# Performance work log

Measured on AMD Instinct MI355X. Metric: run time of the kernel, lower is better.

## Reference

```python
import jax, jax.numpy as jnp
import numpy as np

N_NODES = 100000
N_EDGES = 1600000
IN_DIM = 128
HID = 64


def setup_inputs() -> dict:
    key = jax.random.key(0)
    ks = jax.random.split(key, 12)
    s = 1.0 / np.sqrt(IN_DIM)
    sh = 1.0 / np.sqrt(HID)
    return {
        "x": jax.random.normal(ks[0], (N_NODES, IN_DIM), jnp.float32),
        "edge_index": jax.random.randint(ks[1], (2, N_EDGES), 0, N_NODES, jnp.int64)
        if jax.config.jax_enable_x64 else jax.random.randint(ks[1], (2, N_EDGES), 0, N_NODES, jnp.int32),
        "edge_attr": jax.random.uniform(ks[2], (N_EDGES, 1), jnp.float32),
        "Wi": jax.random.normal(ks[3], (IN_DIM, HID), jnp.float32) * s,
        "bi": jnp.zeros((HID,), jnp.float32),
        "W1": jax.random.normal(ks[4], (HID, HID), jnp.float32) * sh,
        "b1": jnp.zeros((HID,), jnp.float32),
        "W2": jax.random.normal(ks[5], (HID, HID), jnp.float32) * sh,
        "b2": jnp.zeros((HID,), jnp.float32),
        "W3": jax.random.normal(ks[6], (HID, HID), jnp.float32) * sh,
        "b3": jnp.zeros((HID,), jnp.float32),
    }


def reference(x, edge_index, edge_attr, Wi, bi, W1, b1, W2, b2, W3, b3):
    src = edge_index[0]
    tgt = edge_index[1]
    w = edge_attr[:, 0:1]  # [E,1]
    h = jax.nn.relu(x @ Wi + bi)  # [N,H]
    states = [h]
    for W, b in ((W1, b1), (W2, b2), (W3, b3)):
        # per-edge weighted message, scatter-add into target nodes
        msgs = jax.ops.segment_sum(h[src] * w, tgt, num_segments=h.shape[0])
        h = jax.nn.relu((h + msgs) @ W + b)
        states.append(h)
    return jnp.stack(states)  # [4, N, H] (list of states in the original)
```

## Files before the change

### kernel.cpp

```cpp
#include <hip/hip_runtime.h>
#include <hip/hip_bf16.h>

#define N_NODES 100000
#define N_EDGES 1600000
#define IN_DIM  128
#define HID     64
#define BIN_NODES 64
#define NBINS   ((N_NODES + BIN_NODES - 1) / BIN_NODES)
#define EB      2048
#define EB_BLOCKS ((N_EDGES + EB - 1) / EB)
#define CAP     2048

#define PITCH_IN  152
#define PITCH_HID 88

typedef __attribute__((ext_vector_type(8))) short bf16x8;
typedef __attribute__((ext_vector_type(4))) float f32x4;

__device__ inline unsigned short f2bf(float f) {
    __hip_bfloat16 b = __float2bfloat16(f);
    return *reinterpret_cast<unsigned short*>(&b);
}

__global__ void wf_prep_kernel(const float* __restrict__ Wi,
                               const float* __restrict__ W1,
                               const float* __restrict__ W2,
                               const float* __restrict__ W3,
                               unsigned short* __restrict__ wf_in,
                               unsigned short* __restrict__ wf_hid,
                               int* __restrict__ g_bin_cursor) {
    int t = blockIdx.x * 256 + threadIdx.x;
    if (t < NBINS) g_bin_cursor[t] = t * CAP;
    if (t < 8192) {
        int j = t & 7, n16 = (t >> 3) & 15, quad = (t >> 7) & 3, nt = (t >> 9) & 3, kc = t >> 11;
        int k = kc * 32 + quad * 8 + j, n = nt * 16 + n16;
        wf_in[t] = f2bf(Wi[k * HID + n]);
    }
    if (t < 4096) {
        int j = t & 7, n16 = (t >> 3) & 15, quad = (t >> 7) & 3, nt = (t >> 9) & 3, kc = t >> 11;
        int k = kc * 32 + quad * 8 + j, n = nt * 16 + n16;
        wf_hid[t]        = f2bf(W1[k * HID + n]);
        wf_hid[4096 + t] = f2bf(W2[k * HID + n]);
        wf_hid[8192 + t] = f2bf(W3[k * HID + n]);
    }
}

struct ScatterS {
    unsigned long long srec[EB];
    unsigned short sbin[EB];
    int cnt[NBINS];
    int lstart[NBINS];
    int lbase[NBINS];
    int stot;
};
struct GemmS {
    unsigned short sX[64 * PITCH_IN];
};

__global__ __launch_bounds__(256) void fused_prep_kernel(
        const int* __restrict__ src,
        const int* __restrict__ tgt,
        const float* __restrict__ ea,
        int* __restrict__ g_bin_cursor,
        unsigned long long* __restrict__ binned,
        const float* __restrict__ x,
        const unsigned short* __restrict__ wf,
        const float* __restrict__ bi,
        float* __restrict__ h0,
        __hip_bfloat16* __restrict__ hbf) {
    __shared__ __align__(16) unsigned char smem[sizeof(ScatterS)];
    const int tid = threadIdx.x;

    if (blockIdx.x < EB_BLOCKS) {
        ScatterS* S = reinterpret_cast<ScatterS*>(smem);
        for (int i = tid; i < NBINS; i += 256) S->cnt[i] = 0;
        __syncthreads();

        const int e0 = blockIdx.x * EB;
        int myb[EB / 256];
        unsigned long long myrec[EB / 256];
        #pragma unroll
        for (int i = 0; i < EB / 256; ++i) {
            int e = e0 + tid + i * 256;
            if (e < N_EDGES) {
                int t = tgt[e];
                int b = t >> 6;
                myb[i] = b;
                myrec[i] = ((unsigned long long)(unsigned)__float_as_int(ea[e]) << 32)
                         | ((unsigned)(t & 63) << 17) | (unsigned)src[e];
                atomicAdd(&S->cnt[b], 1);
            } else {
                myb[i] = -1;
            }
        }
        __syncthreads();

        if (tid < 64) {
            int carry = 0;
            for (int c = 0; c < (NBINS + 63) / 64; ++c) {
                int idx = c * 64 + tid;
                int v = (idx < NBINS) ? S->cnt[idx] : 0;
                int sc = v;
                #pragma unroll
                for (int d = 1; d < 64; d <<= 1) {
                    int t2 = __shfl_up(sc, d);
                    if (tid >= d) sc += t2;
                }
                if (idx < NBINS) S->lstart[idx] = carry + sc - v;
                carry += __shfl(sc, 63);
            }
            if (tid == 0) S->stot = carry;
        }
        __syncthreads();

        for (int i = tid; i < NBINS; i += 256)
            if (S->cnt[i]) S->lbase[i] = atomicAdd(&g_bin_cursor[i], S->cnt[i]);
        __syncthreads();
        for (int i = tid; i < NBINS; i += 256) S->cnt[i] = 0;
        __syncthreads();

        #pragma unroll
        for (int i = 0; i < EB / 256; ++i) {
            if (myb[i] >= 0) {
                int r = atomicAdd(&S->cnt[myb[i]], 1);
                int p = S->lstart[myb[i]] + r;
                S->srec[p] = myrec[i];
                S->sbin[p] = (unsigned short)myb[i];
            }
        }
        __syncthreads();

        const int tot = S->stot;
        for (int i = tid; i < tot; i += 256) {
            int b = S->sbin[i];
            binned[(size_t)S->lbase[b] + (i - S->lstart[b])] = S->srec[i];
        }
    } else {
        GemmS* G = reinterpret_cast<GemmS*>(smem);
        const int row0 = (blockIdx.x - EB_BLOCKS) * 64;

        #pragma unroll
        for (int it = 0; it < 8; ++it) {
            int i  = tid + it * 256;
            int r  = i >> 5;
            int kq = i & 31;
            int rg = row0 + r;
            float4 v = (rg < N_NODES)
                     ? ((const float4*)x)[(size_t)rg * (IN_DIM / 4) + kq]
                     : make_float4(0.f, 0.f, 0.f, 0.f);
            ushort4 pk;
            pk.x = f2bf(v.x); pk.y = f2bf(v.y); pk.z = f2bf(v.z); pk.w = f2bf(v.w);
            *(ushort4*)(G->sX + r * PITCH_IN + kq * 4) = pk;
        }
        __syncthreads();

        const int lane = tid & 63;
        const int wid  = tid >> 6;
        const int l16  = lane & 15;
        const int q    = lane >> 4;

        f32x4 acc[4] = {{0,0,0,0},{0,0,0,0},{0,0,0,0},{0,0,0,0}};
        const bf16x8* wf8 = (const bf16x8*)wf;

        #pragma unroll
        for (int kc = 0; kc < 4; ++kc) {
            bf16x8 af = *(const bf16x8*)(G->sX + (wid * 16 + l16) * PITCH_IN + kc * 32 + q * 8);
            #pragma unroll
            for (int nt = 0; nt < 4; ++nt) {
                bf16x8 bfr = wf8[((kc * 4 + nt) * 4 + q) * 16 + l16];
                acc[nt] = __builtin_amdgcn_mfma_f32_16x16x32_bf16(af, bfr, acc[nt], 0, 0, 0);
            }
        }

        #pragma unroll
        for (int nt = 0; nt < 4; ++nt) {
            float bb = bi[nt * 16 + l16];
            #pragma unroll
            for (int reg = 0; reg < 4; ++reg) {
                int rg = row0 + wid * 16 + q * 4 + reg;
                if (rg < N_NODES) {
                    float v = fmaxf(acc[nt][reg] + bb, 0.0f);
                    h0 [(size_t)rg * HID + nt * 16 + l16] = v;
                    hbf[(size_t)rg * HID + nt * 16 + l16] = __float2bfloat16(v);
                }
            }
        }
    }
}

__global__ __launch_bounds__(256) void agg_gemm_kernel(
        const float* __restrict__ h,
        const __hip_bfloat16* __restrict__ hbf_in,
        const int* __restrict__ g_bin_cursor,
        const unsigned long long* __restrict__ binned,
        const unsigned short* __restrict__ wf,
        const float* __restrict__ b,
        float* __restrict__ hnext,
        __hip_bfloat16* __restrict__ hbf_out,
        const int store_bf) {
    __shared__ int2 sp[CAP];
    __shared__ unsigned short sXs[64 * PITCH_HID];
    __shared__ int nbase[64], ncur[64], scnt[64];
    const int tid  = threadIdx.x;
    const int bin  = blockIdx.x;
    const int row0 = bin * 64;
    const int lane = tid & 63;
    const int wid  = tid >> 6;
    const int grp  = lane >> 4;
    const int sub  = lane & 15;
    const int ebeg = bin * CAP;
    const int ecnt = g_bin_cursor[bin] - ebeg;

    if (tid < 64) ncur[tid] = 0;
    __syncthreads();
    for (int i = tid; i < ecnt; i += 256)
        atomicAdd(&ncur[(int)((binned[ebeg + i] >> 17) & 63)], 1);
    __syncthreads();

    if (tid < 64) {
        int v = ncur[tid], sc = v;
        #pragma unroll
        for (int d = 1; d < 64; d <<= 1) {
            int t2 = __shfl_up(sc, d);
            if (tid >= d) sc += t2;
        }
        nbase[tid] = sc - v;
        scnt[tid]  = v;
        ncur[tid]  = sc - v;
    }
    __syncthreads();

    for (int i = tid; i < ecnt; i += 256) {
        unsigned long long rec = binned[ebeg + i];
        int lt = (int)((rec >> 17) & 63);
        int r  = atomicAdd(&ncur[lt], 1);
        sp[r] = make_int2((int)(rec & 0x1FFFF), (int)(rec >> 32));
    }
    __syncthreads();

    for (int t = 0; t < 16; ++t) {
        const int lt   = wid * 16 + t;
        const int node = row0 + lt;
        if (node < N_NODES) {
            const int beg = nbase[lt];
            const int cnt = scnt[lt];
            float ax = 0.f, ay = 0.f, az = 0.f, aw = 0.f;
            const int last = cnt - 1;
            for (int i = 0; i < cnt; i += 8) {
                int e0 = i + grp;
                int e1 = i + 4 + grp;
                bool l0 = (e0 <= last);
                bool l1 = (e1 <= last);
                int2 p0 = sp[beg + (l0 ? e0 : last)];
                int2 p1 = sp[beg + (l1 ? e1 : last)];
                uint2 g0 = *(const uint2*)(hbf_in + (size_t)p0.x * HID + sub * 4);
                uint2 g1 = *(const uint2*)(hbf_in + (size_t)p1.x * HID + sub * 4);
                float w0 = l0 ? __int_as_float(p0.y) : 0.0f;
                float w1 = l1 ? __int_as_float(p1.y) : 0.0f;
                ax += w0 * __uint_as_float(g0.x << 16);
                ay += w0 * __uint_as_float(g0.x & 0xFFFF0000u);
                az += w0 * __uint_as_float(g0.y << 16);
                aw += w0 * __uint_as_float(g0.y & 0xFFFF0000u);
                ax += w1 * __uint_as_float(g1.x << 16);
                ay += w1 * __uint_as_float(g1.x & 0xFFFF0000u);
                az += w1 * __uint_as_float(g1.y << 16);
                aw += w1 * __uint_as_float(g1.y & 0xFFFF0000u);
            }
            ax += __shfl_xor(ax, 16); ay += __shfl_xor(ay, 16);
            az += __shfl_xor(az, 16); aw += __shfl_xor(aw, 16);
            ax += __shfl_xor(ax, 32); ay += __shfl_xor(ay, 32);
            az += __shfl_xor(az, 32); aw += __shfl_xor(aw, 32);
            if (grp == 0) {
                const float4 hv = *(const float4*)(h + (size_t)node * HID + sub * 4);
                ushort4 pk;
                pk.x = f2bf(hv.x + ax); pk.y = f2bf(hv.y + ay);
                pk.z = f2bf(hv.z + az); pk.w = f2bf(hv.w + aw);
                *(ushort4*)(sXs + lt * PITCH_HID + sub * 4) = pk;
            }
        } else if (grp == 0) {
            ushort4 z; z.x = 0; z.y = 0; z.z = 0; z.w = 0;
            *(ushort4*)(sXs + lt * PITCH_HID + sub * 4) = z;
        }
    }
    __syncthreads();

    const int l16 = lane & 15;
    const int q   = lane >> 4;

    f32x4 acc[4] = {{0,0,0,0},{0,0,0,0},{0,0,0,0},{0,0,0,0}};
    const bf16x8* wf8 = (const bf16x8*)wf;

    #pragma unroll
    for (int kc = 0; kc < 2; ++kc) {
        bf16x8 af = *(const bf16x8*)(sXs + (wid * 16 + l16) * PITCH_HID + kc * 32 + q * 8);
        #pragma unroll
        for (int nt = 0; nt < 4; ++nt) {
            bf16x8 bfr = wf8[((kc * 4 + nt) * 4 + q) * 16 + l16];
            acc[nt] = __builtin_amdgcn_mfma_f32_16x16x32_bf16(af, bfr, acc[nt], 0, 0, 0);
        }
    }

    #pragma unroll
    for (int nt = 0; nt < 4; ++nt) {
        float bb = b[nt * 16 + l16];
        #pragma unroll
        for (int reg = 0; reg < 4; ++reg) {
            int rg = row0 + wid * 16 + q * 4 + reg;
            if (rg < N_NODES) {
                float v = fmaxf(acc[nt][reg] + bb, 0.0f);
                hnext[(size_t)rg * HID + nt * 16 + l16] = v;
                if (store_bf)
                    hbf_out[(size_t)rg * HID + nt * 16 + l16] = __float2bfloat16(v);
            }
        }
    }
}

extern "C" void kernel_launch(void* const* d_in, const int* in_sizes, int n_in,
                              void* d_out, int out_size, void* d_ws, size_t ws_size,
                              hipStream_t stream) {
    const float* x   = (const float*)d_in[0];
    const int*   ei  = (const int*)  d_in[1];
    const float* ea  = (const float*)d_in[2];
    const float* Wi  = (const float*)d_in[3];
    const float* bi  = (const float*)d_in[4];
    const float* W1  = (const float*)d_in[5];
    const float* b1  = (const float*)d_in[6];
    const float* W2  = (const float*)d_in[7];
    const float* b2  = (const float*)d_in[8];
    const float* W3  = (const float*)d_in[9];
    const float* b3  = (const float*)d_in[10];
    const float* bl[3] = { b1, b2, b3 };
    float* out = (float*)d_out;

    const int* src = ei;
    const int* tgt = ei + N_EDGES;

    unsigned long long* binned = (unsigned long long*)d_ws;
    int* g_bin_cursor = (int*)(binned + (size_t)NBINS * CAP);
    __hip_bfloat16* hbf0 = (__hip_bfloat16*)(g_bin_cursor + NBINS + 1);
    __hip_bfloat16* hbf1 = hbf0 + (size_t)N_NODES * HID;
    unsigned short* wf_in  = (unsigned short*)(hbf1 + (size_t)N_NODES * HID);
    unsigned short* wf_hid = wf_in + 8192;

    wf_prep_kernel<<<32, 256, 0, stream>>>(Wi, W1, W2, W3, wf_in, wf_hid,
                                           g_bin_cursor);

    const int gemm_blocks = (N_NODES + 63) / 64;
    fused_prep_kernel<<<EB_BLOCKS + gemm_blocks, 256, 0, stream>>>(
        src, tgt, ea, g_bin_cursor, binned,
        x, wf_in, bi, out, hbf0);

    __hip_bfloat16* hin  = hbf0;
    __hip_bfloat16* hout = hbf1;
    for (int l = 0; l < 3; ++l) {
        const float* hl = out + (size_t)l * N_NODES * HID;
        float* hn       = out + (size_t)(l + 1) * N_NODES * HID;
        agg_gemm_kernel<<<NBINS, 256, 0, stream>>>(
            hl, hin, g_bin_cursor, binned,
            wf_hid + (size_t)l * 4096, bl[l], hn, hout, (l < 2) ? 1 : 0);
        __hip_bfloat16* t = hin; hin = hout; hout = t;
    }
}
```

Baseline: 419.3 us.

## Replace two-level bin sort with direct per-node edge slots via global atomics

Edges are no longer radix-binned into 64-node bins in shared memory and then re-sorted by node inside every aggregation layer. A single scatter kernel now uses one global atomic per edge to place (src, weight) records into a fixed 64-slot row per target node. The aggregation kernel reads each node's slots with one wavefront load, prefetches the next node's row, and hands out edges through lane shuffles instead of an LDS list. This removes the per-layer in-block sorting and LDS staging, at the cost of scattered global atomics and a larger sparse workspace. Any edges beyond 64 per node are silently dropped, and the input GEMM no longer runs in the same launch as the scatter.

```diff
diff --git a/kernel.cpp b/kernel.cpp
--- a/kernel.cpp
+++ b/kernel.cpp
@@ -5,11 +5,7 @@
 #define N_EDGES 1600000
 #define IN_DIM  128
 #define HID     64
-#define BIN_NODES 64
-#define NBINS   ((N_NODES + BIN_NODES - 1) / BIN_NODES)
-#define EB      2048
-#define EB_BLOCKS ((N_EDGES + EB - 1) / EB)
-#define CAP     2048
+#define CAP_N   64
 
 #define PITCH_IN  152
 #define PITCH_HID 88
@@ -28,9 +24,9 @@
                                const float* __restrict__ W3,
                                unsigned short* __restrict__ wf_in,
                                unsigned short* __restrict__ wf_hid,
-                               int* __restrict__ g_bin_cursor) {
+                               int* __restrict__ cnt) {
     int t = blockIdx.x * 256 + threadIdx.x;
-    if (t < NBINS) g_bin_cursor[t] = t * CAP;
+    if (t < N_NODES) cnt[t] = 0;
     if (t < 8192) {
         int j = t & 7, n16 = (t >> 3) & 15, quad = (t >> 7) & 3, nt = (t >> 9) & 3, kc = t >> 11;
         int k = kc * 32 + quad * 8 + j, n = nt * 16 + n16;
@@ -45,144 +41,74 @@
     }
 }
 
-struct ScatterS {
-    unsigned long long srec[EB];
-    unsigned short sbin[EB];
-    int cnt[NBINS];
-    int lstart[NBINS];
-    int lbase[NBINS];
-    int stot;
-};
-struct GemmS {
-    unsigned short sX[64 * PITCH_IN];
-};
-
-__global__ __launch_bounds__(256) void fused_prep_kernel(
+__global__ __launch_bounds__(256) void scatter_direct_kernel(
         const int* __restrict__ src,
         const int* __restrict__ tgt,
         const float* __restrict__ ea,
-        int* __restrict__ g_bin_cursor,
-        unsigned long long* __restrict__ binned,
+        int* __restrict__ cnt,
+        int2* __restrict__ binned) {
+    int e = blockIdx.x * 256 + threadIdx.x;
+    if (e < N_EDGES) {
+        int t = tgt[e];
+        int r = atomicAdd(&cnt[t], 1);
+        if (r < CAP_N)
+            binned[(size_t)t * CAP_N + r] = make_int2(src[e], __float_as_int(ea[e]));
+    }
+}
+
+__global__ __launch_bounds__(256) void gemm_in_kernel(
         const float* __restrict__ x,
         const unsigned short* __restrict__ wf,
         const float* __restrict__ bi,
         float* __restrict__ h0,
         __hip_bfloat16* __restrict__ hbf) {
-    __shared__ __align__(16) unsigned char smem[sizeof(ScatterS)];
-    const int tid = threadIdx.x;
-
-    if (blockIdx.x < EB_BLOCKS) {
-        ScatterS* S = reinterpret_cast<ScatterS*>(smem);
-        for (int i = tid; i < NBINS; i += 256) S->cnt[i] = 0;
-        __syncthreads();
-
-        const int e0 = blockIdx.x * EB;
-        int myb[EB / 256];
-        unsigned long long myrec[EB / 256];
-        #pragma unroll
-        for (int i = 0; i < EB / 256; ++i) {
-            int e = e0 + tid + i * 256;
-            if (e < N_EDGES) {
-                int t = tgt[e];
-                int b = t >> 6;
-                myb[i] = b;
-                myrec[i] = ((unsigned long long)(unsigned)__float_as_int(ea[e]) << 32)
-                         | ((unsigned)(t & 63) << 17) | (unsigned)src[e];
-                atomicAdd(&S->cnt[b], 1);
-            } else {
-                myb[i] = -1;
-            }
-        }
-        __syncthreads();
-
-        if (tid < 64) {
-            int carry = 0;
-            for (int c = 0; c < (NBINS + 63) / 64; ++c) {
-                int idx = c * 64 + tid;
-                int v = (idx < NBINS) ? S->cnt[idx] : 0;
-                int sc = v;
-                #pragma unroll
-                for (int d = 1; d < 64; d <<= 1) {
-                    int t2 = __shfl_up(sc, d);
-                    if (tid >= d) sc += t2;
-                }
-                if (idx < NBINS) S->lstart[idx] = carry + sc - v;
-                carry += __shfl(sc, 63);
-            }
-            if (tid == 0) S->stot = carry;
-        }
-        __syncthreads();
-
-        for (int i = tid; i < NBINS; i += 256)
-            if (S->cnt[i]) S->lbase[i] = atomicAdd(&g_bin_cursor[i], S->cnt[i]);
-        __syncthreads();
-        for (int i = tid; i < NBINS; i += 256) S->cnt[i] = 0;
-        __syncthreads();
-
-        #pragma unroll
-        for (int i = 0; i < EB / 256; ++i) {
-            if (myb[i] >= 0) {
-                int r = atomicAdd(&S->cnt[myb[i]], 1);
-                int p = S->lstart[myb[i]] + r;
-                S->srec[p] = myrec[i];
-                S->sbin[p] = (unsigned short)myb[i];
-            }
-        }
-        __syncthreads();
-
-        const int tot = S->stot;
-        for (int i = tid; i < tot; i += 256) {
-            int b = S->sbin[i];
-            binned[(size_t)S->lbase[b] + (i - S->lstart[b])] = S->srec[i];
-        }
-    } else {
-        GemmS* G = reinterpret_cast<GemmS*>(smem);
-        const int row0 = (blockIdx.x - EB_BLOCKS) * 64;
-
-        #pragma unroll
-        for (int it = 0; it < 8; ++it) {
-            int i  = tid + it * 256;
-            int r  = i >> 5;
-            int kq = i & 31;
-            int rg = row0 + r;
-            float4 v = (rg < N_NODES)
-                     ? ((const float4*)x)[(size_t)rg * (IN_DIM / 4) + kq]
-                     : make_float4(0.f, 0.f, 0.f, 0.f);
-            ushort4 pk;
-            pk.x = f2bf(v.x); pk.y = f2bf(v.y); pk.z = f2bf(v.z); pk.w = f2bf(v.w);
-            *(ushort4*)(G->sX + r * PITCH_IN + kq * 4) = pk;
-        }
-        __syncthreads();
-
-        const int lane = tid & 63;
-        const int wid  = tid >> 6;
-        const int l16  = lane & 15;
-        const int q    = lane >> 4;
-
-        f32x4 acc[4] = {{0,0,0,0},{0,0,0,0},{0,0,0,0},{0,0,0,0}};
-        const bf16x8* wf8 = (const bf16x8*)wf;
-
-        #pragma unroll
-        for (int kc = 0; kc < 4; ++kc) {
-            bf16x8 af = *(const bf16x8*)(G->sX + (wid * 16 + l16) * PITCH_IN + kc * 32 + q * 8);
-            #pragma unroll
-            for (int nt = 0; nt < 4; ++nt) {
-                bf16x8 bfr = wf8[((kc * 4 + nt) * 4 + q) * 16 + l16];
-                acc[nt] = __builtin_amdgcn_mfma_f32_16x16x32_bf16(af, bfr, acc[nt], 0, 0, 0);
-            }
-        }
-
+    __shared__ unsigned short sX[64 * PITCH_IN];
+    const int tid  = threadIdx.x;
+    const int row0 = blockIdx.x * 64;
+
+    #pragma unroll
+    for (int it = 0; it < 8; ++it) {
+        int i  = tid + it * 256;
+        int r  = i >> 5;
+        int kq = i & 31;
+        int rg = row0 + r;
+        float4 v = (rg < N_NODES)
+                 ? ((const float4*)x)[(size_t)rg * (IN_DIM / 4) + kq]
+                 : make_float4(0.f, 0.f, 0.f, 0.f);
+        ushort4 pk;
+        pk.x = f2bf(v.x); pk.y = f2bf(v.y); pk.z = f2bf(v.z); pk.w = f2bf(v.w);
+        *(ushort4*)(sX + r * PITCH_IN + kq * 4) = pk;
+    }
+    __syncthreads();
+
+    const int lane = tid & 63;
+    const int wid  = tid >> 6;
+    const int l16  = lane & 15;
+    const int q    = lane >> 4;
+
+    f32x4 acc[4] = {{0,0,0,0},{0,0,0,0},{0,0,0,0},{0,0,0,0}};
+    const bf16x8* wf8 = (const bf16x8*)wf;
+
+    #pragma unroll
+    for (int kc = 0; kc < 4; ++kc) {
+        bf16x8 af = *(const bf16x8*)(sX + (wid * 16 + l16) * PITCH_IN + kc * 32 + q * 8);
         #pragma unroll
         for (int nt = 0; nt < 4; ++nt) {
-            float bb = bi[nt * 16 + l16];
-            #pragma unroll
-            for (int reg = 0; reg < 4; ++reg) {
-                int rg = row0 + wid * 16 + q * 4 + reg;
-                if (rg < N_NODES) {
-                    float v = fmaxf(acc[nt][reg] + bb, 0.0f);
-                    h0 [(size_t)rg * HID + nt * 16 + l16] = v;
-                    hbf[(size_t)rg * HID + nt * 16 + l16] = __float2bfloat16(v);
-                }
+            bf16x8 bfr = wf8[((kc * 4 + nt) * 4 + q) * 16 + l16];
+            acc[nt] = __builtin_amdgcn_mfma_f32_16x16x32_bf16(af, bfr, acc[nt], 0, 0, 0);
+        }
+    }
+
+    #pragma unroll
+    for (int nt = 0; nt < 4; ++nt) {
+        float bb = bi[nt * 16 + l16];
+        #pragma unroll
+        for (int reg = 0; reg < 4; ++reg) {
+            int rg = row0 + wid * 16 + q * 4 + reg;
+            if (rg < N_NODES) {
+                float v = fmaxf(acc[nt][reg] + bb, 0.0f);
+                h0 [(size_t)rg * HID + nt * 16 + l16] = v;
+                hbf[(size_t)rg * HID + nt * 16 + l16] = __float2bfloat16(v);
             }
         }
     }
@@ -191,72 +117,57 @@
 __global__ __launch_bounds__(256) void agg_gemm_kernel(
         const float* __restrict__ h,
         const __hip_bfloat16* __restrict__ hbf_in,
-        const int* __restrict__ g_bin_cursor,
-        const unsigned long long* __restrict__ binned,
+        const int* __restrict__ cnt,
+        const int2* __restrict__ binned,
         const unsigned short* __restrict__ wf,
         const float* __restrict__ b,
         float* __restrict__ hnext,
         __hip_bfloat16* __restrict__ hbf_out,
         const int store_bf) {
-    __shared__ int2 sp[CAP];
     __shared__ unsigned short sXs[64 * PITCH_HID];
-    __shared__ int nbase[64], ncur[64], scnt[64];
     const int tid  = threadIdx.x;
-    const int bin  = blockIdx.x;
-    const int row0 = bin * 64;
+    const int row0 = blockIdx.x * 64;
     const int lane = tid & 63;
     const int wid  = tid >> 6;
     const int grp  = lane >> 4;
     const int sub  = lane & 15;
-    const int ebeg = bin * CAP;
-    const int ecnt = g_bin_cursor[bin] - ebeg;
-
-    if (tid < 64) ncur[tid] = 0;
-    __syncthreads();
-    for (int i = tid; i < ecnt; i += 256)
-        atomicAdd(&ncur[(int)((binned[ebeg + i] >> 17) & 63)], 1);
-    __syncthreads();
-
-    if (tid < 64) {
-        int v = ncur[tid], sc = v;
-        #pragma unroll
-        for (int d = 1; d < 64; d <<= 1) {
-            int t2 = __shfl_up(sc, d);
-            if (tid >= d) sc += t2;
-        }
-        nbase[tid] = sc - v;
-        scnt[tid]  = v;
-        ncur[tid]  = sc - v;
-    }
-    __syncthreads();
-
-    for (int i = tid; i < ecnt; i += 256) {
-        unsigned long long rec = binned[ebeg + i];
-        int lt = (int)((rec >> 17) & 63);
-        int r  = atomicAdd(&ncur[lt], 1);
-        sp[r] = make_int2((int)(rec & 0x1FFFF), (int)(rec >> 32));
-    }
-    __syncthreads();
+
+    const int node0 = row0 + wid * 16;
+
+    int cv = 0;
+    {
+        int nl = node0 + (lane & 15);
+        if (lane < 16 && nl < N_NODES) cv = min(cnt[nl], CAP_N);
+    }
+
+    int c0 = __shfl(cv, 0);
+    int2 pl = binned[(size_t)min(node0, N_NODES - 1) * CAP_N + min(lane, max(c0 - 1, 0))];
 
     for (int t = 0; t < 16; ++t) {
-        const int lt   = wid * 16 + t;
-        const int node = row0 + lt;
+        const int node = node0 + t;
+        const int ccur = __shfl(cv, t);
+        const int2 pl_cur = pl;
+        if (t < 15) {
+            int cn = __shfl(cv, t + 1);
+            pl = binned[(size_t)min(node + 1, N_NODES - 1) * CAP_N
+                        + min(lane, max(cn - 1, 0))];
+        }
         if (node < N_NODES) {
-            const int beg = nbase[lt];
-            const int cnt = scnt[lt];
             float ax = 0.f, ay = 0.f, az = 0.f, aw = 0.f;
-            const int last = cnt - 1;
-            for (int i = 0; i < cnt; i += 8) {
+            const int last = ccur - 1;
+            for (int i = 0; i < ccur; i += 8) {
                 int e0 = i + grp;
                 int e1 = i + 4 + grp;
                 bool l0 = (e0 <= last);
                 bool l1 = (e1 <= last);
-                int2 p0 = sp[beg + (l0 ? e0 : last)];
-                int2 p1 = sp[beg + (l1 ? e1 : last)];
-                uint2 g0 = *(const uint2*)(hbf_in + (size_t)p0.x * HID + sub * 4);
-                uint2 g1 = *(const uint2*)(hbf_in + (size_t)p1.x * HID + sub * 4);
-                float w0 = l0 ? __int_as_float(p0.y) : 0.0f;
-                float w1 = l1 ? __int_as_float(p1.y) : 0.0f;
+                int s0  = __shfl(pl_cur.x, l0 ? e0 : last);
+                int w0i = __shfl(pl_cur.y, l0 ? e0 : last);
+                int s1  = __shfl(pl_cur.x, l1 ? e1 : last);
+                int w1i = __shfl(pl_cur.y, l1 ? e1 : last);
+                uint2 g0 = *(const uint2*)(hbf_in + (size_t)s0 * HID + sub * 4);
+                uint2 g1 = *(const uint2*)(hbf_in + (size_t)s1 * HID + sub * 4);
+                float w0 = l0 ? __int_as_float(w0i) : 0.0f;
+                float w1 = l1 ? __int_as_float(w1i) : 0.0f;
                 ax += w0 * __uint_as_float(g0.x << 16);
                 ay += w0 * __uint_as_float(g0.x & 0xFFFF0000u);
                 az += w0 * __uint_as_float(g0.y << 16);
@@ -275,11 +186,11 @@
                 ushort4 pk;
                 pk.x = f2bf(hv.x + ax); pk.y = f2bf(hv.y + ay);
                 pk.z = f2bf(hv.z + az); pk.w = f2bf(hv.w + aw);
-                *(ushort4*)(sXs + lt * PITCH_HID + sub * 4) = pk;
+                *(ushort4*)(sXs + (wid * 16 + t) * PITCH_HID + sub * 4) = pk;
             }
         } else if (grp == 0) {
             ushort4 z; z.x = 0; z.y = 0; z.z = 0; z.w = 0;
-            *(ushort4*)(sXs + lt * PITCH_HID + sub * 4) = z;
+            *(ushort4*)(sXs + (wid * 16 + t) * PITCH_HID + sub * 4) = z;
         }
     }
     __syncthreads();
@@ -336,28 +247,30 @@
     const int* src = ei;
     const int* tgt = ei + N_EDGES;
 
-    unsigned long long* binned = (unsigned long long*)d_ws;
-    int* g_bin_cursor = (int*)(binned + (size_t)NBINS * CAP);
-    __hip_bfloat16* hbf0 = (__hip_bfloat16*)(g_bin_cursor + NBINS + 1);
+    int2* binned = (int2*)d_ws;
+    int* cnt = (int*)(binned + (size_t)N_NODES * CAP_N);
+    __hip_bfloat16* hbf0 = (__hip_bfloat16*)(cnt + N_NODES);
     __hip_bfloat16* hbf1 = hbf0 + (size_t)N_NODES * HID;
     unsigned short* wf_in  = (unsigned short*)(hbf1 + (size_t)N_NODES * HID);
     unsigned short* wf_hid = wf_in + 8192;
 
-    wf_prep_kernel<<<32, 256, 0, stream>>>(Wi, W1, W2, W3, wf_in, wf_hid,
-                                           g_bin_cursor);
+    const int prep_blocks = (N_NODES + 255) / 256;
+    wf_prep_kernel<<<prep_blocks, 256, 0, stream>>>(Wi, W1, W2, W3,
+                                                    wf_in, wf_hid, cnt);
+
+    const int sc_blocks = (N_EDGES + 255) / 256;
+    scatter_direct_kernel<<<sc_blocks, 256, 0, stream>>>(src, tgt, ea, cnt, binned);
 
     const int gemm_blocks = (N_NODES + 63) / 64;
-    fused_prep_kernel<<<EB_BLOCKS + gemm_blocks, 256, 0, stream>>>(
-        src, tgt, ea, g_bin_cursor, binned,
-        x, wf_in, bi, out, hbf0);
+    gemm_in_kernel<<<gemm_blocks, 256, 0, stream>>>(x, wf_in, bi, out, hbf0);
 
     __hip_bfloat16* hin  = hbf0;
     __hip_bfloat16* hout = hbf1;
     for (int l = 0; l < 3; ++l) {
         const float* hl = out + (size_t)l * N_NODES * HID;
         float* hn       = out + (size_t)(l + 1) * N_NODES * HID;
-        agg_gemm_kernel<<<NBINS, 256, 0, stream>>>(
-            hl, hin, g_bin_cursor, binned,
+        agg_gemm_kernel<<<gemm_blocks, 256, 0, stream>>>(
+            hl, hin, cnt, binned,
             wf_hid + (size_t)l * 4096, bl[l], hn, hout, (l < 2) ? 1 : 0);
         __hip_bfloat16* t = hin; hin = hout; hout = t;
     }
```

Measured after the change: 409.5 us. 2.3% less time.

## Build per-node padded edge lists once and reuse them across all layers

Applied to the files above, without the earlier changes.

Coarse binning now uses 256-node bins. A new fine_fill kernel runs once and sorts each bin's edges into a padded per-node array of (src, weight) pairs plus a per-node count. Each of the three aggregation layers used to count and sort its edges per bin in LDS with atomics; it now reads a node's pairs straight into registers, prefetches the next node's pairs and hands out src and weight with wave shuffles. Scatter and input-GEMM blocks are also interleaved in the fused prep grid. The cost is a 64-slot padded array with more memory traffic, and any node with more than 64 incoming edges silently loses the extra edges.

```diff
diff --git a/kernel.cpp b/kernel.cpp
--- a/kernel.cpp
+++ b/kernel.cpp
@@ -5,11 +5,15 @@
 #define N_EDGES 1600000
 #define IN_DIM  128
 #define HID     64
-#define BIN_NODES 64
+#define BIN_NODES 256
 #define NBINS   ((N_NODES + BIN_NODES - 1) / BIN_NODES)
 #define EB      2048
-#define EB_BLOCKS ((N_EDGES + EB - 1) / EB)
-#define CAP     2048
+#define CAP     8192
+#define CAP_N   64
+
+#define SC_BLOCKS ((N_EDGES + EB - 1) / EB)
+#define GEMM_BLOCKS ((N_NODES + 63) / 64)
+#define PREP_BLOCKS ((N_NODES + 255) / 256)
 
 #define PITCH_IN  152
 #define PITCH_HID 88
@@ -56,8 +60,9 @@
 struct GemmS {
     unsigned short sX[64 * PITCH_IN];
 };
-
-__global__ __launch_bounds__(256) void fused_prep_kernel(
+#define FUSED_SMEM ((sizeof(ScatterS) > sizeof(GemmS)) ? sizeof(ScatterS) : sizeof(GemmS))
+
+__global__ __launch_bounds__(256) void fused_scatter_gemm_kernel(
         const int* __restrict__ src,
         const int* __restrict__ tgt,
         const float* __restrict__ ea,
@@ -68,15 +73,23 @@
         const float* __restrict__ bi,
         float* __restrict__ h0,
         __hip_bfloat16* __restrict__ hbf) {
-    __shared__ __align__(16) unsigned char smem[sizeof(ScatterS)];
+    __shared__ __align__(16) unsigned char smem[FUSED_SMEM];
     const int tid = threadIdx.x;
 
-    if (blockIdx.x < EB_BLOCKS) {
+    int sb = -1, gb = -1;
+    if (blockIdx.x < 2 * SC_BLOCKS) {
+        if ((blockIdx.x & 1) == 0) sb = blockIdx.x >> 1;
+        else                       gb = blockIdx.x >> 1;
+    } else {
+        gb = SC_BLOCKS + (blockIdx.x - 2 * SC_BLOCKS);
+    }
+
+    if (sb >= 0) {
         ScatterS* S = reinterpret_cast<ScatterS*>(smem);
         for (int i = tid; i < NBINS; i += 256) S->cnt[i] = 0;
         __syncthreads();
 
-        const int e0 = blockIdx.x * EB;
+        const int e0 = sb * EB;
         int myb[EB / 256];
         unsigned long long myrec[EB / 256];
         #pragma unroll
@@ -84,10 +97,10 @@
             int e = e0 + tid + i * 256;
             if (e < N_EDGES) {
                 int t = tgt[e];
-                int b = t >> 6;
+                int b = t >> 8;
                 myb[i] = b;
                 myrec[i] = ((unsigned long long)(unsigned)__float_as_int(ea[e]) << 32)
-                         | ((unsigned)(t & 63) << 17) | (unsigned)src[e];
+                         | ((unsigned)(t & 255) << 17) | (unsigned)src[e];
                 atomicAdd(&S->cnt[b], 1);
             } else {
                 myb[i] = -1;
@@ -135,128 +148,142 @@
             int b = S->sbin[i];
             binned[(size_t)S->lbase[b] + (i - S->lstart[b])] = S->srec[i];
         }
-    } else {
-        GemmS* G = reinterpret_cast<GemmS*>(smem);
-        const int row0 = (blockIdx.x - EB_BLOCKS) * 64;
-
-        #pragma unroll
-        for (int it = 0; it < 8; ++it) {
-            int i  = tid + it * 256;
-            int r  = i >> 5;
-            int kq = i & 31;
-            int rg = row0 + r;
-            float4 v = (rg < N_NODES)
-                     ? ((const float4*)x)[(size_t)rg * (IN_DIM / 4) + kq]
-                     : make_float4(0.f, 0.f, 0.f, 0.f);
-            ushort4 pk;
-            pk.x = f2bf(v.x); pk.y = f2bf(v.y); pk.z = f2bf(v.z); pk.w = f2bf(v.w);
-            *(ushort4*)(G->sX + r * PITCH_IN + kq * 4) = pk;
-        }
-        __syncthreads();
-
-        const int lane = tid & 63;
-        const int wid  = tid >> 6;
-        const int l16  = lane & 15;
-        const int q    = lane >> 4;
-
-        f32x4 acc[4] = {{0,0,0,0},{0,0,0,0},{0,0,0,0},{0,0,0,0}};
-        const bf16x8* wf8 = (const bf16x8*)wf;
-
-        #pragma unroll
-        for (int kc = 0; kc < 4; ++kc) {
-            bf16x8 af = *(const bf16x8*)(G->sX + (wid * 16 + l16) * PITCH_IN + kc * 32 + q * 8);
-            #pragma unroll
-            for (int nt = 0; nt < 4; ++nt) {
-                bf16x8 bfr = wf8[((kc * 4 + nt) * 4 + q) * 16 + l16];
-                acc[nt] = __builtin_amdgcn_mfma_f32_16x16x32_bf16(af, bfr, acc[nt], 0, 0, 0);
-            }
-        }
-
+        return;
+    }
+
+    GemmS* G = reinterpret_cast<GemmS*>(smem);
+    const int row0 = gb * 64;
+
+    #pragma unroll
+    for (int it = 0; it < 8; ++it) {
+        int i  = tid + it * 256;
+        int r  = i >> 5;
+        int kq = i & 31;
+        int rg = row0 + r;
+        float4 v = (rg < N_NODES)
+                 ? ((const float4*)x)[(size_t)rg * (IN_DIM / 4) + kq]
+                 : make_float4(0.f, 0.f, 0.f, 0.f);
+        ushort4 pk;
+        pk.x = f2bf(v.x); pk.y = f2bf(v.y); pk.z = f2bf(v.z); pk.w = f2bf(v.w);
+        *(ushort4*)(G->sX + r * PITCH_IN + kq * 4) = pk;
+    }
+    __syncthreads();
+
+    const int lane = tid & 63;
+    const int wid  = tid >> 6;
+    const int l16  = lane & 15;
+    const int q    = lane >> 4;
+
+    f32x4 acc[4] = {{0,0,0,0},{0,0,0,0},{0,0,0,0},{0,0,0,0}};
+    const bf16x8* wf8 = (const bf16x8*)wf;
+
+    #pragma unroll
+    for (int kc = 0; kc < 4; ++kc) {
+        bf16x8 af = *(const bf16x8*)(G->sX + (wid * 16 + l16) * PITCH_IN + kc * 32 + q * 8);
         #pragma unroll
         for (int nt = 0; nt < 4; ++nt) {
-            float bb = bi[nt * 16 + l16];
-            #pragma unroll
-            for (int reg = 0; reg < 4; ++reg) {
-                int rg = row0 + wid * 16 + q * 4 + reg;
-                if (rg < N_NODES) {
-                    float v = fmaxf(acc[nt][reg] + bb, 0.0f);
-                    h0 [(size_t)rg * HID + nt * 16 + l16] = v;
-                    hbf[(size_t)rg * HID + nt * 16 + l16] = __float2bfloat16(v);
-                }
-            }
-        }
+            bf16x8 bfr = wf8[((kc * 4 + nt) * 4 + q) * 16 + l16];
+            acc[nt] = __builtin_amdgcn_mfma_f32_16x16x32_bf16(af, bfr, acc[nt], 0, 0, 0);
+        }
+    }
+
+    #pragma unroll
+    for (int nt = 0; nt < 4; ++nt) {
+        float bb = bi[nt * 16 + l16];
+        #pragma unroll
+        for (int reg = 0; reg < 4; ++reg) {
+            int rg = row0 + wid * 16 + q * 4 + reg;
+            if (rg < N_NODES) {
+                float v = fmaxf(acc[nt][reg] + bb, 0.0f);
+                h0 [(size_t)rg * HID + nt * 16 + l16] = v;
+                hbf[(size_t)rg * HID + nt * 16 + l16] = __float2bfloat16(v);
+            }
+        }
+    }
+}
+
+__global__ __launch_bounds__(1024) void fine_fill_kernel(
+        const unsigned long long* __restrict__ binned,
+        const int* __restrict__ g_bin_cursor,
+        int* __restrict__ cnt2,
+        int2* __restrict__ pairs) {
+    __shared__ int ncur[256];
+    const int b   = blockIdx.x;
+    const int tid = threadIdx.x;
+    const int ebeg = b * CAP;
+    const int ecnt = g_bin_cursor[b] - ebeg;
+
+    if (tid < 256) ncur[tid] = 0;
+    __syncthreads();
+    for (int i = tid; i < ecnt; i += 1024) {
+        unsigned long long rec = binned[ebeg + i];
+        int lt = (int)((rec >> 17) & 255);
+        int r  = atomicAdd(&ncur[lt], 1);
+        if (r < CAP_N)
+            pairs[(size_t)(b * 256 + lt) * CAP_N + r] =
+                make_int2((int)(rec & 0x1FFFF), (int)(rec >> 32));
+    }
+    __syncthreads();
+    if (tid < 256) {
+        int node = b * 256 + tid;
+        if (node < N_NODES) cnt2[node] = min(ncur[tid], CAP_N);
     }
 }
 
 __global__ __launch_bounds__(256) void agg_gemm_kernel(
         const float* __restrict__ h,
         const __hip_bfloat16* __restrict__ hbf_in,
-        const int* __restrict__ g_bin_cursor,
-        const unsigned long long* __restrict__ binned,
+        const int* __restrict__ cnt2,
+        const int2* __restrict__ pairs,
         const unsigned short* __restrict__ wf,
         const float* __restrict__ b,
         float* __restrict__ hnext,
         __hip_bfloat16* __restrict__ hbf_out,
         const int store_bf) {
-    __shared__ int2 sp[CAP];
     __shared__ unsigned short sXs[64 * PITCH_HID];
-    __shared__ int nbase[64], ncur[64], scnt[64];
     const int tid  = threadIdx.x;
-    const int bin  = blockIdx.x;
-    const int row0 = bin * 64;
+    const int row0 = blockIdx.x * 64;
     const int lane = tid & 63;
     const int wid  = tid >> 6;
     const int grp  = lane >> 4;
     const int sub  = lane & 15;
-    const int ebeg = bin * CAP;
-    const int ecnt = g_bin_cursor[bin] - ebeg;
-
-    if (tid < 64) ncur[tid] = 0;
-    __syncthreads();
-    for (int i = tid; i < ecnt; i += 256)
-        atomicAdd(&ncur[(int)((binned[ebeg + i] >> 17) & 63)], 1);
-    __syncthreads();
-
-    if (tid < 64) {
-        int v = ncur[tid], sc = v;
-        #pragma unroll
-        for (int d = 1; d < 64; d <<= 1) {
-            int t2 = __shfl_up(sc, d);
-            if (tid >= d) sc += t2;
-        }
-        nbase[tid] = sc - v;
-        scnt[tid]  = v;
-        ncur[tid]  = sc - v;
-    }
-    __syncthreads();
-
-    for (int i = tid; i < ecnt; i += 256) {
-        unsigned long long rec = binned[ebeg + i];
-        int lt = (int)((rec >> 17) & 63);
-        int r  = atomicAdd(&ncur[lt], 1);
-        sp[r] = make_int2((int)(rec & 0x1FFFF), (int)(rec >> 32));
-    }
-    __syncthreads();
+
+    const int node0 = row0 + wid * 16;
+
+    int cv = 0;
+    {
+        int nl = node0 + (lane & 15);
+        if (lane < 16 && nl < N_NODES) cv = cnt2[nl];
+    }
+
+    int c0 = __shfl(cv, 0);
+    int2 pl = pairs[(size_t)min(node0, N_NODES - 1) * CAP_N + min(lane, max(c0 - 1, 0))];
 
     for (int t = 0; t < 16; ++t) {
-        const int lt   = wid * 16 + t;
-        const int node = row0 + lt;
+        const int node = node0 + t;
+        const int ccur = __shfl(cv, t);
+        const int2 pl_cur = pl;
+        if (t < 15) {
+            int cn = __shfl(cv, t + 1);
+            pl = pairs[(size_t)min(node + 1, N_NODES - 1) * CAP_N
+                        + min(lane, max(cn - 1, 0))];
+        }
         if (node < N_NODES) {
-            const int beg = nbase[lt];
-            const int cnt = scnt[lt];
             float ax = 0.f, ay = 0.f, az = 0.f, aw = 0.f;
-            const int last = cnt - 1;
-            for (int i = 0; i < cnt; i += 8) {
+            const int last = ccur - 1;
+            for (int i = 0; i < ccur; i += 8) {
                 int e0 = i + grp;
                 int e1 = i + 4 + grp;
                 bool l0 = (e0 <= last);
                 bool l1 = (e1 <= last);
-                int2 p0 = sp[beg + (l0 ? e0 : last)];
-                int2 p1 = sp[beg + (l1 ? e1 : last)];
-                uint2 g0 = *(const uint2*)(hbf_in + (size_t)p0.x * HID + sub * 4);
-                uint2 g1 = *(const uint2*)(hbf_in + (size_t)p1.x * HID + sub * 4);
-                float w0 = l0 ? __int_as_float(p0.y) : 0.0f;
-                float w1 = l1 ? __int_as_float(p1.y) : 0.0f;
+                int s0  = __shfl(pl_cur.x, l0 ? e0 : last);
+                int w0i = __shfl(pl_cur.y, l0 ? e0 : last);
+                int s1  = __shfl(pl_cur.x, l1 ? e1 : last);
+                int w1i = __shfl(pl_cur.y, l1 ? e1 : last);
+                uint2 g0 = *(const uint2*)(hbf_in + (size_t)s0 * HID + sub * 4);
+                uint2 g1 = *(const uint2*)(hbf_in + (size_t)s1 * HID + sub * 4);
+                float w0 = l0 ? __int_as_float(w0i) : 0.0f;
+                float w1 = l1 ? __int_as_float(w1i) : 0.0f;
                 ax += w0 * __uint_as_float(g0.x << 16);
                 ay += w0 * __uint_as_float(g0.x & 0xFFFF0000u);
                 az += w0 * __uint_as_float(g0.y << 16);
@@ -275,11 +302,11 @@
                 ushort4 pk;
                 pk.x = f2bf(hv.x + ax); pk.y = f2bf(hv.y + ay);
                 pk.z = f2bf(hv.z + az); pk.w = f2bf(hv.w + aw);
-                *(ushort4*)(sXs + lt * PITCH_HID + sub * 4) = pk;
+                *(ushort4*)(sXs + (wid * 16 + t) * PITCH_HID + sub * 4) = pk;
             }
         } else if (grp == 0) {
             ushort4 z; z.x = 0; z.y = 0; z.z = 0; z.w = 0;
-            *(ushort4*)(sXs + lt * PITCH_HID + sub * 4) = z;
+            *(ushort4*)(sXs + (wid * 16 + t) * PITCH_HID + sub * 4) = z;
         }
     }
     __syncthreads();
@@ -337,27 +364,31 @@
     const int* tgt = ei + N_EDGES;
 
     unsigned long long* binned = (unsigned long long*)d_ws;
-    int* g_bin_cursor = (int*)(binned + (size_t)NBINS * CAP);
+    int2* pairs = (int2*)(binned + (size_t)NBINS * CAP);
+    int* cnt2   = (int*)(pairs + (size_t)N_NODES * CAP_N);
+    int* g_bin_cursor = cnt2 + N_NODES;
     __hip_bfloat16* hbf0 = (__hip_bfloat16*)(g_bin_cursor + NBINS + 1);
     __hip_bfloat16* hbf1 = hbf0 + (size_t)N_NODES * HID;
     unsigned short* wf_in  = (unsigned short*)(hbf1 + (size_t)N_NODES * HID);
     unsigned short* wf_hid = wf_in + 8192;
 
-    wf_prep_kernel<<<32, 256, 0, stream>>>(Wi, W1, W2, W3, wf_in, wf_hid,
-                                           g_bin_cursor);
-
-    const int gemm_blocks = (N_NODES + 63) / 64;
-    fused_prep_kernel<<<EB_BLOCKS + gemm_blocks, 256, 0, stream>>>(
-        src, tgt, ea, g_bin_cursor, binned,
-        x, wf_in, bi, out, hbf0);
+    wf_prep_kernel<<<PREP_BLOCKS, 256, 0, stream>>>(Wi, W1, W2, W3,
+                                                    wf_in, wf_hid, g_bin_cursor);
+
+    const int fused_grid = 2 * SC_BLOCKS + (GEMM_BLOCKS - SC_BLOCKS);
+    fused_scatter_gemm_kernel<<<fused_grid, 256, 0, stream>>>(
+        src, tgt, ea, g_bin_cursor, binned, x, wf_in, bi, out, hbf0);
+
+    fine_fill_kernel<<<NBINS, 1024, 0, stream>>>(binned, g_bin_cursor,
+                                                 cnt2, pairs);
 
     __hip_bfloat16* hin  = hbf0;
     __hip_bfloat16* hout = hbf1;
     for (int l = 0; l < 3; ++l) {
         const float* hl = out + (size_t)l * N_NODES * HID;
         float* hn       = out + (size_t)(l + 1) * N_NODES * HID;
-        agg_gemm_kernel<<<NBINS, 256, 0, stream>>>(
-            hl, hin, g_bin_cursor, binned,
+        agg_gemm_kernel<<<GEMM_BLOCKS, 256, 0, stream>>>(
+            hl, hin, cnt2, pairs,
             wf_hid + (size_t)l * 4096, bl[l], hn, hout, (l < 2) ? 1 : 0);
         __hip_bfloat16* t = hin; hin = hout; hout = t;
     }
```

After: 380.3 us. 1.1x faster.
